# Performance work log

Hardware: AMD Instinct MI355X
Metric: run time of the kernel (lower is better)

The kernel has to match this reference:

```python
import jax, jax.numpy as jnp
import numpy as np

ALPHA = 0.2   # LeakyReLU slope from source
HEADS = 8

def _proj(x, W, s, b):
    # Conv3D(kernel=1, no bias) + fused inference BatchNorm affine + LeakyReLU
    y = jnp.einsum('nchwd,de->nchwe', x, W) * s + b
    return jnp.where(y >= 0, y, ALPHA * y)

def setup_inputs() -> dict:
    key = jax.random.key(0)
    ks = jax.random.split(key, 13)
    N, D, H, W, C = 2, 64, 64, 64, 64   # D == in_channels (axis 1), C is last axis
    KC, VC = 64, 64
    p = lambda k, sh, sc=0.1: jax.random.normal(k, sh, jnp.float32) * sc
    return {
        'x':  jax.random.normal(ks[0], (N, D, H, W, C), jnp.float32),
        'Wk': p(ks[1], (D, KC)), 'sk': 1.0 + p(ks[2], (KC,)), 'bk': p(ks[3], (KC,)),
        'Wq': p(ks[4], (D, KC)), 'sq': 1.0 + p(ks[5], (KC,)), 'bq': p(ks[6], (KC,)),
        'Wv': p(ks[7], (D, VC)), 'sv': 1.0 + p(ks[8], (VC,)), 'bv': p(ks[9], (VC,)),
        'Wr': p(ks[10], (VC, D)), 'sr': 1.0 + p(ks[11], (D,)), 'br': p(ks[12], (D,)),
    }

def reference(x, Wk, sk, bk, Wq, sq, bq, Wv, sv, bv, Wr, sr, br):
    n, d, h, w, c = x.shape
    xt = jnp.transpose(x, (0, 4, 2, 3, 1))            # (n, c, h, w, d)
    keys    = _proj(xt, Wk, sk, bk)                   # (n, c, h, w, KC)
    queries = _proj(xt, Wq, sq, bq)
    values  = _proj(xt, Wv, sv, bv)
    T = c * h * w
    KC, VC = Wk.shape[1], Wv.shape[1]
    hk, hv = KC // HEADS, VC // HEADS                 # hk == hv required by source math
    K = jax.nn.softmax(keys.reshape(n, T, HEADS, hk), axis=1)      # softmax over tokens
    Q = jax.nn.softmax(queries.reshape(n, T, HEADS, hk), axis=-1)  # softmax over head channels
    V = values.reshape(n, T, HEADS, hv)
    ctx = jnp.einsum('ntak,ntav->nakv', K, V)         # (n, heads, hk, hv) small context
    # source: tf.matmul(context, query^T) contracts ctx's hv with query's hk axis
    att = jnp.einsum('nakv,ntav->nakt', ctx, Q)       # (n, heads, hk, T)
    # faithful raw reshape per head (n, hk, T) -> (n, c, h, w, hv), heads concat last
    att = att.reshape(n, HEADS, c, h, w, hv)
    agg = jnp.transpose(att, (0, 2, 3, 4, 1, 5)).reshape(n, c, h, w, HEADS * hv)
    rep = _proj(agg, Wr, sr, br)                      # (n, c, h, w, d)
    return x + jnp.transpose(rep, (0, 4, 2, 3, 1))
```

## Files before the change

### kernel.cpp

```cpp
#include <hip/hip_runtime.h>

#define ALPHA 0.2f

__device__ float g_part[8192 * 576];
__device__ float g_red[2 * 32 * 1024];
__device__ float g_ctx[1024];

__global__ __launch_bounds__(256) void k_kv(
    const float* __restrict__ x,
    const float* __restrict__ Wk, const float* __restrict__ sk, const float* __restrict__ bk,
    const float* __restrict__ Wv, const float* __restrict__ sv, const float* __restrict__ bv)
{
  __shared__ __align__(16) float sh[12288];
  float* xt = sh;
  float* WL = sh + 4096;

  const int tid = threadIdx.x;
  const int bid = blockIdx.x;
  const int n  = bid >> 12;
  const int hw = bid & 4095;

  const float* xrow = x + (size_t)n * 16777216u + (size_t)hw * 64u;

  #pragma unroll
  for (int i = 0; i < 4; ++i) {
    int idx = tid + i * 256;
    int d = idx >> 4, c4 = (idx & 15) * 4;
    *(float4*)&xt[d * 64 + c4] = *(const float4*)(xrow + (size_t)d * 262144u + c4);
  }
  #pragma unroll
  for (int i = 0; i < 8; ++i) {
    int idx = tid + i * 256;
    int d = idx >> 5, e4 = (idx & 31) * 4;
    const float* src = (e4 < 64) ? (Wk + d * 64 + e4) : (Wv + d * 64 + e4 - 64);
    *(float4*)&WL[d * 128 + e4] = *(const float4*)src;
  }
  __syncthreads();

  const int tok0 = (tid & 15) * 4;
  const int eg   = tid >> 4;
  const int e0   = eg * 8;

  float acc[4][8];
  #pragma unroll
  for (int t = 0; t < 4; ++t)
    #pragma unroll
    for (int j = 0; j < 8; ++j) acc[t][j] = 0.f;

  #pragma unroll 4
  for (int d = 0; d < 64; ++d) {
    float4 xv = *(const float4*)&xt[d * 64 + tok0];
    float4 wa = *(const float4*)&WL[d * 128 + e0];
    float4 wb = *(const float4*)&WL[d * 128 + e0 + 4];
    float xr[4] = {xv.x, xv.y, xv.z, xv.w};
    float w[8]  = {wa.x, wa.y, wa.z, wa.w, wb.x, wb.y, wb.z, wb.w};
    #pragma unroll
    for (int t = 0; t < 4; ++t)
      #pragma unroll
      for (int j = 0; j < 8; ++j) acc[t][j] += xr[t] * w[j];
  }

  const bool isK = (eg < 8);
  const int  ec  = isK ? e0 : (e0 - 64);
  const float* sp = (isK ? sk : sv) + ec;
  const float* bp = (isK ? bk : bv) + ec;
  float s8[8], b8[8];
  *(float4*)&s8[0] = *(const float4*)(sp);
  *(float4*)&s8[4] = *(const float4*)(sp + 4);
  *(float4*)&b8[0] = *(const float4*)(bp);
  *(float4*)&b8[4] = *(const float4*)(bp + 4);

  __syncthreads();

  float* eK = sh;
  float* vV = sh + 4160;
  float* dst = (isK ? eK : vV) + ec;
  #pragma unroll
  for (int t = 0; t < 4; ++t) {
    #pragma unroll
    for (int j = 0; j < 8; ++j) {
      float y = acc[t][j] * s8[j] + b8[j];
      y = (y >= 0.f) ? y : ALPHA * y;
      if (isK) y = __expf(fminf(y, 60.f));
      dst[(tok0 + t) * 65 + j] = y;
    }
  }
  __syncthreads();

  {
    float* pE = sh + 8320;
    float* pS = sh + 8320 + 256;
    const int ch = tid & 63;
    const int tq = tid >> 6;
    const int a8 = ch & ~7;

    float E = 0.f;
    float S[8];
    #pragma unroll
    for (int v = 0; v < 8; ++v) S[v] = 0.f;
    for (int t = tq * 16; t < tq * 16 + 16; ++t) {
      float e = eK[t * 65 + ch];
      E += e;
      #pragma unroll
      for (int v = 0; v < 8; ++v) S[v] += e * vV[t * 65 + a8 + v];
    }
    pE[tq * 64 + ch] = E;
    #pragma unroll
    for (int v = 0; v < 8; ++v) pS[(tq * 64 + ch) * 8 + v] = S[v];
    __syncthreads();

    if (tid < 64) {
      float* gp = g_part + (size_t)bid * 576u;
      float E4 = pE[tid] + pE[64 + tid] + pE[128 + tid] + pE[192 + tid];
      gp[tid] = E4;
      #pragma unroll
      for (int v = 0; v < 8; ++v) {
        float S4 = pS[tid * 8 + v] + pS[(64 + tid) * 8 + v]
                 + pS[(128 + tid) * 8 + v] + pS[(192 + tid) * 8 + v];
        gp[64 + v * 64 + tid] = S4;
      }
    }
  }
}

__global__ __launch_bounds__(256) void k_red() {
  const int ob = blockIdx.x & 3;
  const int bc = blockIdx.x >> 2;
  const int i  = ob * 256 + threadIdx.x;
  const int n = i >> 9, ch = (i & 511) >> 3, v = i & 7;
  const float* base = g_part + ((size_t)n * 4096u + (size_t)bc * 128u) * 576u;
  float l = 0.f, S = 0.f;
  #pragma unroll 8
  for (int b = 0; b < 128; ++b) {
    l += base[(size_t)b * 576u + ch];
    S += base[(size_t)b * 576u + 64u + (size_t)v * 64u + ch];
  }
  g_red[bc * 1024 + i]         = l;
  g_red[32768 + bc * 1024 + i] = S;
}

__global__ __launch_bounds__(256) void k_ctx() {
  int i = blockIdx.x * 256 + threadIdx.x;
  if (i >= 1024) return;
  float l = 0.f, S = 0.f;
  #pragma unroll
  for (int r = 0; r < 32; ++r) {
    l += g_red[r * 1024 + i];
    S += g_red[32768 + r * 1024 + i];
  }
  float c = (l > 0.f) ? (S / l) : 0.f;
  if (!(__builtin_fabsf(c) < 1e30f)) c = 0.f;
  g_ctx[i] = c;
}

__global__ __launch_bounds__(256) void k_att(
    const float* __restrict__ x,
    const float* __restrict__ Wq, const float* __restrict__ sq, const float* __restrict__ bq,
    const float* __restrict__ Wr, const float* __restrict__ sr, const float* __restrict__ br,
    float* __restrict__ out)
{
  __shared__ __align__(16) float WqL[64 * 64];
  __shared__ __align__(16) float xw[64 * 64];
  __shared__ float qL[64 * 65];
  __shared__ float aggL[64 * 65];
  __shared__ float ctxL[64 * 9];
  __shared__ float srL[64], brL[64];

  const int tid = threadIdx.x;
  const int bid = blockIdx.x;
  const int n  = bid >> 12;
  const int hwp = bid & 4095;
  const int hp = hwp >> 6, wp = hwp & 63;

  const int jc    = hp >> 3;
  const int h_t   = (hp & 7) * 8 + (wp >> 3);
  const int wbase = (wp & 7) * 8;

  #pragma unroll
  for (int i = 0; i < 4; ++i) {
    int idx = tid + i * 256;
    int r = idx >> 4, c4 = (idx & 15) * 4;
    *(float4*)&WqL[r * 64 + c4] = *(const float4*)(Wq + r * 64 + c4);
  }
  if (tid < 64) { srL[tid] = sr[tid]; brL[tid] = br[tid]; }

  for (int i = tid; i < 512; i += 256) {
    int ch = i >> 3, v = i & 7;
    ctxL[ch * 9 + v] = g_ctx[n * 512 + ch * 8 + v];
  }

  {
    const size_t xb = (size_t)n * 16777216u + (size_t)h_t * 4096u;
    #pragma unroll
    for (int i = 0; i < 16; ++i) {
      int idx = tid + i * 256;
      int d = idx >> 6, tok = idx & 63;
      int vpp = tok >> 3, cl = tok & 7;
      xw[d * 64 + tok] = x[xb + (size_t)d * 262144u + (size_t)(wbase + vpp) * 64u + (cl * 8 + jc)];
    }
  }
  __syncthreads();

  {
    const int tok0 = (tid & 31) * 2;
    const int ch0  = (tid >> 5) * 8;
    float acc0[8], acc1[8];
    #pragma unroll
    for (int j = 0; j < 8; ++j) { acc0[j] = 0.f; acc1[j] = 0.f; }
    #pragma unroll 4
    for (int d = 0; d < 64; ++d) {
      float2 xv = *(const float2*)&xw[d * 64 + tok0];
      float4 wa = *(const float4*)&WqL[d * 64 + ch0];
      float4 wb = *(const float4*)&WqL[d * 64 + ch0 + 4];
      float w[8] = {wa.x, wa.y, wa.z, wa.w, wb.x, wb.y, wb.z, wb.w};
      #pragma unroll
      for (int j = 0; j < 8; ++j) { acc0[j] += xv.x * w[j]; acc1[j] += xv.y * w[j]; }
    }
    float sv8[8], bv8[8];
    *(float4*)&sv8[0] = *(const float4*)(sq + ch0);
    *(float4*)&sv8[4] = *(const float4*)(sq + ch0 + 4);
    *(float4*)&bv8[0] = *(const float4*)(bq + ch0);
    *(float4*)&bv8[4] = *(const float4*)(bq + ch0 + 4);
    #pragma unroll
    for (int i = 0; i < 2; ++i) {
      float* a = (i == 0) ? acc0 : acc1;
      float mx = -3.0e38f;
      #pragma unroll
      for (int j = 0; j < 8; ++j) {
        float y = a[j] * sv8[j] + bv8[j];
        y = (y >= 0.f) ? y : ALPHA * y;
        a[j] = y;
        mx = fmaxf(mx, y);
      }
      float sum = 0.f;
      #pragma unroll
      for (int j = 0; j < 8; ++j) { a[j] = __expf(a[j] - mx); sum += a[j]; }
      float inv = 1.f / sum;
      #pragma unroll
      for (int j = 0; j < 8; ++j) qL[(tok0 + i) * 65 + ch0 + j] = a[j] * inv;
    }
  }
  __syncthreads();

  #pragma unroll
  for (int i = 0; i < 4; ++i) {
    int idx = tid + i * 256;
    int r = idx >> 4, c4 = (idx & 15) * 4;
    *(float4*)&xw[r * 64 + c4] = *(const float4*)(Wr + r * 64 + c4);
  }

  {
    const int cp = tid & 63, eb = tid >> 6;
    const int kk = cp >> 3, cl = cp & 7;
    #pragma unroll
    for (int je = 0; je < 16; ++je) {
      int e = eb * 16 + je;
      int a = e >> 3, vpp = e & 7;
      const float* cx = &ctxL[(a * 8 + kk) * 9];
      const float* qr = &qL[(vpp * 8 + cl) * 65 + a * 8];
      float s = 0.f;
      #pragma unroll
      for (int v = 0; v < 8; ++v) s += cx[v] * qr[v];
      aggL[cp * 65 + e] = s;
    }
  }
  __syncthreads();

  {
    const int ci = tid & 63, dq = tid >> 6;
    float accr[16];
    #pragma unroll
    for (int i = 0; i < 16; ++i) accr[i] = 0.f;
    #pragma unroll 4
    for (int e = 0; e < 64; ++e) {
      float av = aggL[ci * 65 + e];
      const float* wr = &xw[e * 64 + dq * 16];
      #pragma unroll
      for (int i = 0; i < 16; ++i) accr[i] += av * wr[i];
    }
    const size_t xb = (size_t)n * 16777216u + (size_t)hwp * 64u + (size_t)ci;
    #pragma unroll
    for (int i = 0; i < 16; ++i) {
      int di = dq * 16 + i;
      float y = accr[i] * srL[di] + brL[di];
      y = (y >= 0.f) ? y : ALPHA * y;
      out[xb + (size_t)di * 262144u] = x[xb + (size_t)di * 262144u] + y;
    }
  }
}

extern "C" void kernel_launch(void* const* d_in, const int* in_sizes, int n_in,
                              void* d_out, int out_size, void* d_ws, size_t ws_size,
                              hipStream_t stream)
{
  (void)in_sizes; (void)n_in; (void)out_size; (void)d_ws; (void)ws_size;

  const float* x  = (const float*)d_in[0];
  const float* Wk = (const float*)d_in[1];
  const float* sk = (const float*)d_in[2];
  const float* bk = (const float*)d_in[3];
  const float* Wq = (const float*)d_in[4];
  const float* sq = (const float*)d_in[5];
  const float* bq = (const float*)d_in[6];
  const float* Wv = (const float*)d_in[7];
  const float* sv = (const float*)d_in[8];
  const float* bv = (const float*)d_in[9];
  const float* Wr = (const float*)d_in[10];
  const float* sr = (const float*)d_in[11];
  const float* br = (const float*)d_in[12];
  float* out = (float*)d_out;

  k_kv  <<<dim3(8192), dim3(256), 0, stream>>>(x, Wk, sk, bk, Wv, sv, bv);
  k_red <<<dim3(128),  dim3(256), 0, stream>>>();
  k_ctx <<<dim3(4),    dim3(256), 0, stream>>>();
  k_att <<<dim3(8192), dim3(256), 0, stream>>>(x, Wq, sq, bq, Wr, sr, br, out);
}
```

Before: 598.6 us.

## Use direct global-to-LDS loads, vectorized LDS layouts, and XCD-aware block remap

Replaces register-staged global loads of x, weights and Wq/Wr with global_load_lds direct-to-LDS transfers and hoists the scale/bias loads ahead of the barrier. Shared buffers are re-padded (stride 68, rotated q rows, ctx stride 12) so intermediate writes and reads become float4 LDS accesses with fewer bank conflicts, and aggL now reuses the Wq buffer to cut LDS footprint. The attention kernel remaps block indices so that blocks sharing the same XCD work on neighbouring tiles, aiming at better L2 locality. The risks are the less-tested LDS DMA path and the more involved index math.

```diff
diff --git a/kernel.cpp b/kernel.cpp
--- a/kernel.cpp
+++ b/kernel.cpp
@@ -1,6 +1,9 @@
 #include <hip/hip_runtime.h>
 
 #define ALPHA 0.2f
+
+typedef const __attribute__((address_space(1))) unsigned int gu32;
+typedef __attribute__((address_space(3))) unsigned int lu32;
 
 __device__ float g_part[8192 * 576];
 __device__ float g_red[2 * 32 * 1024];
@@ -26,20 +29,32 @@
   for (int i = 0; i < 4; ++i) {
     int idx = tid + i * 256;
     int d = idx >> 4, c4 = (idx & 15) * 4;
-    *(float4*)&xt[d * 64 + c4] = *(const float4*)(xrow + (size_t)d * 262144u + c4);
+    __builtin_amdgcn_global_load_lds((gu32*)(xrow + (size_t)d * 262144u + c4),
+                                     (lu32*)&xt[idx * 4], 16, 0, 0);
   }
   #pragma unroll
   for (int i = 0; i < 8; ++i) {
     int idx = tid + i * 256;
     int d = idx >> 5, e4 = (idx & 31) * 4;
     const float* src = (e4 < 64) ? (Wk + d * 64 + e4) : (Wv + d * 64 + e4 - 64);
-    *(float4*)&WL[d * 128 + e4] = *(const float4*)src;
-  }
-  __syncthreads();
+    __builtin_amdgcn_global_load_lds((gu32*)src, (lu32*)&WL[idx * 4], 16, 0, 0);
+  }
 
   const int tok0 = (tid & 15) * 4;
   const int eg   = tid >> 4;
   const int e0   = eg * 8;
+  const bool isK = (eg < 8);
+  const int  ec  = isK ? e0 : (e0 - 64);
+
+  const float* sp = (isK ? sk : sv) + ec;
+  const float* bp = (isK ? bk : bv) + ec;
+  float s8[8], b8[8];
+  *(float4*)&s8[0] = *(const float4*)(sp);
+  *(float4*)&s8[4] = *(const float4*)(sp + 4);
+  *(float4*)&b8[0] = *(const float4*)(bp);
+  *(float4*)&b8[4] = *(const float4*)(bp + 4);
+
+  __syncthreads();
 
   float acc[4][8];
   #pragma unroll
@@ -60,36 +75,29 @@
       for (int j = 0; j < 8; ++j) acc[t][j] += xr[t] * w[j];
   }
 
-  const bool isK = (eg < 8);
-  const int  ec  = isK ? e0 : (e0 - 64);
-  const float* sp = (isK ? sk : sv) + ec;
-  const float* bp = (isK ? bk : bv) + ec;
-  float s8[8], b8[8];
-  *(float4*)&s8[0] = *(const float4*)(sp);
-  *(float4*)&s8[4] = *(const float4*)(sp + 4);
-  *(float4*)&b8[0] = *(const float4*)(bp);
-  *(float4*)&b8[4] = *(const float4*)(bp + 4);
-
   __syncthreads();
 
   float* eK = sh;
-  float* vV = sh + 4160;
-  float* dst = (isK ? eK : vV) + ec;
+  float* vV = sh + 4352;
+  float* dst = (isK ? eK : vV);
   #pragma unroll
   for (int t = 0; t < 4; ++t) {
+    float y8[8];
     #pragma unroll
     for (int j = 0; j < 8; ++j) {
       float y = acc[t][j] * s8[j] + b8[j];
       y = (y >= 0.f) ? y : ALPHA * y;
       if (isK) y = __expf(fminf(y, 60.f));
-      dst[(tok0 + t) * 65 + j] = y;
-    }
-  }
-  __syncthreads();
-
-  {
-    float* pE = sh + 8320;
-    float* pS = sh + 8320 + 256;
+      y8[j] = y;
+    }
+    *(float4*)&dst[(tok0 + t) * 68 + ec]     = *(float4*)&y8[0];
+    *(float4*)&dst[(tok0 + t) * 68 + ec + 4] = *(float4*)&y8[4];
+  }
+  __syncthreads();
+
+  {
+    float* pE = sh + 8704;
+    float* pS = sh + 8960;
     const int ch = tid & 63;
     const int tq = tid >> 6;
     const int a8 = ch & ~7;
@@ -99,10 +107,12 @@
     #pragma unroll
     for (int v = 0; v < 8; ++v) S[v] = 0.f;
     for (int t = tq * 16; t < tq * 16 + 16; ++t) {
-      float e = eK[t * 65 + ch];
+      float e = eK[t * 68 + ch];
+      float4 v0 = *(const float4*)&vV[t * 68 + a8];
+      float4 v1 = *(const float4*)&vV[t * 68 + a8 + 4];
       E += e;
-      #pragma unroll
-      for (int v = 0; v < 8; ++v) S[v] += e * vV[t * 65 + a8 + v];
+      S[0] += e * v0.x; S[1] += e * v0.y; S[2] += e * v0.z; S[3] += e * v0.w;
+      S[4] += e * v1.x; S[5] += e * v1.y; S[6] += e * v1.z; S[7] += e * v1.w;
     }
     pE[tq * 64 + ch] = E;
     #pragma unroll
@@ -159,34 +169,39 @@
     const float* __restrict__ Wr, const float* __restrict__ sr, const float* __restrict__ br,
     float* __restrict__ out)
 {
-  __shared__ __align__(16) float WqL[64 * 64];
+  __shared__ __align__(16) float WqA[64 * 65];
   __shared__ __align__(16) float xw[64 * 64];
-  __shared__ float qL[64 * 65];
-  __shared__ float aggL[64 * 65];
-  __shared__ float ctxL[64 * 9];
+  __shared__ __align__(16) float qL[64 * 64];
+  __shared__ __align__(16) float ctxL[64 * 12];
   __shared__ float srL[64], brL[64];
 
   const int tid = threadIdx.x;
-  const int bid = blockIdx.x;
-  const int n  = bid >> 12;
-  const int hwp = bid & 4095;
-  const int hp = hwp >> 6, wp = hwp & 63;
-
-  const int jc    = hp >> 3;
-  const int h_t   = (hp & 7) * 8 + (wp >> 3);
+  const int lin = blockIdx.x;
+
+  const int xcd   = lin & 7;
+  const int jc    = (lin >> 3) & 7;
+  const int rest  = lin >> 6;
+  const int combo = rest * 8 + xcd;
+  const int n     = combo >> 9;
+  const int hp_lo = (combo >> 6) & 7;
+  const int wp    = combo & 63;
+  const int hp    = jc * 8 + hp_lo;
+  const int hwp   = hp * 64 + wp;
+
+  const int h_t   = hp_lo * 8 + (wp >> 3);
   const int wbase = (wp & 7) * 8;
 
   #pragma unroll
   for (int i = 0; i < 4; ++i) {
     int idx = tid + i * 256;
-    int r = idx >> 4, c4 = (idx & 15) * 4;
-    *(float4*)&WqL[r * 64 + c4] = *(const float4*)(Wq + r * 64 + c4);
+    __builtin_amdgcn_global_load_lds((gu32*)(Wq + idx * 4),
+                                     (lu32*)&WqA[idx * 4], 16, 0, 0);
   }
   if (tid < 64) { srL[tid] = sr[tid]; brL[tid] = br[tid]; }
 
   for (int i = tid; i < 512; i += 256) {
     int ch = i >> 3, v = i & 7;
-    ctxL[ch * 9 + v] = g_ctx[n * 512 + ch * 8 + v];
+    ctxL[ch * 12 + v] = g_ctx[n * 512 + ch * 8 + v];
   }
 
   {
@@ -210,8 +225,8 @@
     #pragma unroll 4
     for (int d = 0; d < 64; ++d) {
       float2 xv = *(const float2*)&xw[d * 64 + tok0];
-      float4 wa = *(const float4*)&WqL[d * 64 + ch0];
-      float4 wb = *(const float4*)&WqL[d * 64 + ch0 + 4];
+      float4 wa = *(const float4*)&WqA[d * 64 + ch0];
+      float4 wb = *(const float4*)&WqA[d * 64 + ch0 + 4];
       float w[8] = {wa.x, wa.y, wa.z, wa.w, wb.x, wb.y, wb.z, wb.w};
       #pragma unroll
       for (int j = 0; j < 8; ++j) { acc0[j] += xv.x * w[j]; acc1[j] += xv.y * w[j]; }
@@ -236,8 +251,13 @@
       #pragma unroll
       for (int j = 0; j < 8; ++j) { a[j] = __expf(a[j] - mx); sum += a[j]; }
       float inv = 1.f / sum;
-      #pragma unroll
-      for (int j = 0; j < 8; ++j) qL[(tok0 + i) * 65 + ch0 + j] = a[j] * inv;
+      float o8[8];
+      #pragma unroll
+      for (int j = 0; j < 8; ++j) o8[j] = a[j] * inv;
+      const int t = tok0 + i;
+      const int rot = (4 * t) & 63;
+      *(float4*)&qL[t * 64 + ((ch0 + rot) & 63)]     = *(float4*)&o8[0];
+      *(float4*)&qL[t * 64 + ((ch0 + 4 + rot) & 63)] = *(float4*)&o8[4];
     }
   }
   __syncthreads();
@@ -245,28 +265,33 @@
   #pragma unroll
   for (int i = 0; i < 4; ++i) {
     int idx = tid + i * 256;
-    int r = idx >> 4, c4 = (idx & 15) * 4;
-    *(float4*)&xw[r * 64 + c4] = *(const float4*)(Wr + r * 64 + c4);
-  }
-
-  {
+    __builtin_amdgcn_global_load_lds((gu32*)(Wr + idx * 4),
+                                     (lu32*)&xw[idx * 4], 16, 0, 0);
+  }
+
+  {
+    float* aggL = WqA;
     const int cp = tid & 63, eb = tid >> 6;
     const int kk = cp >> 3, cl = cp & 7;
     #pragma unroll
     for (int je = 0; je < 16; ++je) {
       int e = eb * 16 + je;
       int a = e >> 3, vpp = e & 7;
-      const float* cx = &ctxL[(a * 8 + kk) * 9];
-      const float* qr = &qL[(vpp * 8 + cl) * 65 + a * 8];
-      float s = 0.f;
-      #pragma unroll
-      for (int v = 0; v < 8; ++v) s += cx[v] * qr[v];
+      float4 c0 = *(const float4*)&ctxL[(a * 8 + kk) * 12];
+      float4 c1 = *(const float4*)&ctxL[(a * 8 + kk) * 12 + 4];
+      int t = vpp * 8 + cl;
+      int rot = (4 * t) & 63;
+      float4 q0 = *(const float4*)&qL[t * 64 + ((a * 8 + rot) & 63)];
+      float4 q1 = *(const float4*)&qL[t * 64 + ((a * 8 + 4 + rot) & 63)];
+      float s = q0.x * c0.x + q0.y * c0.y + q0.z * c0.z + q0.w * c0.w
+              + q1.x * c1.x + q1.y * c1.y + q1.z * c1.z + q1.w * c1.w;
       aggL[cp * 65 + e] = s;
     }
   }
   __syncthreads();
 
   {
+    const float* aggL = WqA;
     const int ci = tid & 63, dq = tid >> 6;
     float accr[16];
     #pragma unroll
```

New measurement: 496.3 us. -17.1%, faster.
